# Performance work log

Measured on AMD Instinct MI355X. Metric: run time of the kernel, lower is better.

The kernel has to match this reference:

```python
import jax, jax.numpy as jnp
import numpy as np
import math

B, S, D, H, DFF = 16, 1024, 512, 8, 2048
DH = D // H
EPS = 1e-5


def setup_inputs() -> dict:
    key = jax.random.key(0)
    ks = jax.random.split(key, 16)
    sc = 0.02
    inp = {
        "x": jax.random.normal(ks[0], (B, S, D), dtype=jnp.float32),
        "mask": jnp.zeros((B, 1, 1, S), dtype=jnp.float32),
        # attention projections (stored as [in, out])
        "wq": jax.random.normal(ks[1], (D, D), jnp.float32) * sc,
        "bq": jnp.zeros((D,), jnp.float32),
        "wk": jax.random.normal(ks[2], (D, D), jnp.float32) * sc,
        "bk": jnp.zeros((D,), jnp.float32),
        "wv": jax.random.normal(ks[3], (D, D), jnp.float32) * sc,
        "bv": jnp.zeros((D,), jnp.float32),
        "wo": jax.random.normal(ks[4], (D, D), jnp.float32) * sc,
        "bo": jnp.zeros((D,), jnp.float32),
        # FFN
        "w1": jax.random.normal(ks[5], (D, DFF), jnp.float32) * sc,
        "b1": jnp.zeros((DFF,), jnp.float32),
        "w2": jax.random.normal(ks[6], (DFF, D), jnp.float32) * sc,
        "b2": jnp.zeros((D,), jnp.float32),
        # LayerNorms over the full [S, D] slab (normalized_shape=[S, D])
        "ln1_w": jnp.ones((S, D), jnp.float32),
        "ln1_b": jnp.zeros((S, D), jnp.float32),
        "ln2_w": jnp.ones((S, D), jnp.float32),
        "ln2_b": jnp.zeros((S, D), jnp.float32),
    }
    return inp


def _layernorm_2d(x, w, b):
    # torch nn.LayerNorm([S, D]): normalize jointly over last two dims
    m = jnp.mean(x, axis=(-2, -1), keepdims=True)
    v = jnp.mean(jnp.square(x - m), axis=(-2, -1), keepdims=True)
    return (x - m) * jax.lax.rsqrt(v + EPS) * w + b


def _encoder_layer(x, mask, wq, bq, wk, bk, wv, bv, wo, bo,
                   w1, b1, w2, b2, ln1_w, ln1_b, ln2_w, ln2_b):
    # --- multi-head attention ---
    def heads(t):  # [B,S,D] -> [B,H,S,DH]
        return t.reshape(B, S, H, DH).transpose(0, 2, 1, 3)

    q = heads(x @ wq + bq)
    k = heads(x @ wk + bk)
    v = heads(x @ wv + bv)

    logits = jnp.einsum("bhqd,bhkd->bhqk", q, k) / math.sqrt(DH)
    logits = logits + mask * -1e9
    attn = jax.nn.softmax(logits, axis=-1)          # [B,H,S,S]
    ctx = jnp.einsum("bhqk,bhkd->bhqd", attn, v)    # [B,H,S,DH]
    ctx = ctx.transpose(0, 2, 1, 3).reshape(B, S, D)
    attn_out = ctx @ wo + bo

    out1 = _layernorm_2d(x + attn_out, ln1_w, ln1_b)

    # --- FFN ---
    ffn = jax.nn.relu(out1 @ w1 + b1) @ w2 + b2
    out2 = _layernorm_2d(out1 + ffn, ln2_w, ln2_b)
    return out2


def reference(x, mask, wq, bq, wk, bk, wv, bv, wo, bo,
              w1, b1, w2, b2, ln1_w, ln1_b, ln2_w, ln2_b):
    return _encoder_layer(x, mask, wq, bq, wk, bk, wv, bv, wo, bo,
                          w1, b1, w2, b2, ln1_w, ln1_b, ln2_w, ln2_b)
```

## Files before the change

kernel.cpp:

```cpp
#include <hip/hip_runtime.h>
#include <stdint.h>

#define B_   16
#define S_   1024
#define D_   512
#define H_   8
#define DH_  64
#define DFF_ 2048
#define M_   (B_*S_)
#define SD_  (S_*D_)
#define NT_  16

typedef unsigned short u16;
typedef unsigned int u32;
typedef __attribute__((ext_vector_type(2))) unsigned int u32x2;
typedef __attribute__((ext_vector_type(4))) unsigned short u16x4;
typedef __attribute__((ext_vector_type(8))) short bf16x8;
typedef __attribute__((ext_vector_type(4))) float f32x4;
typedef __attribute__((ext_vector_type(16))) float f32x16;

#define LOG2E 1.4426950408889634f

#if defined(__has_builtin)
#if __has_builtin(__builtin_amdgcn_permlane32_swap)
#define HAVE_PLS 1
#endif
#endif

__device__ __forceinline__ u16 f2bf(float f) {
  union { float f; uint32_t u; } x{f};
  uint32_t r = x.u + 0x7fffu + ((x.u >> 16) & 1u);
  return (u16)(r >> 16);
}

__device__ __forceinline__ float bf2f(u16 v) {
  union { uint32_t u; float f; } x{(uint32_t)v << 16};
  return x.f;
}

__device__ __forceinline__ u32 pk2(float lo, float hi) {
  union { float f; u32 u; } a{lo}, b{hi};
  return __builtin_amdgcn_perm(b.u, a.u, 0x07060302u);
}

__device__ __forceinline__ float exp2fast(float x) {
#if __has_builtin(__builtin_amdgcn_exp2f)
  return __builtin_amdgcn_exp2f(x);
#else
  return exp2f(x);
#endif
}

__device__ __forceinline__ void gload16(const u16* g, u16* l) {
  __builtin_amdgcn_global_load_lds(
      (const __attribute__((address_space(1))) uint32_t*)g,
      (__attribute__((address_space(3))) uint32_t*)l, 16, 0, 0);
}

__device__ __forceinline__ int swz3(int r) { return (r & 7) ^ ((r >> 3) & 7); }

__global__ __launch_bounds__(256) void prep_kernel(
    const float* __restrict__ x, u16* __restrict__ xb,
    const float* __restrict__ wq, const float* __restrict__ wk,
    const float* __restrict__ wv, const float* __restrict__ wo,
    const float* __restrict__ w1, const float* __restrict__ w2,
    u16* __restrict__ wqkvT, u16* __restrict__ woT,
    u16* __restrict__ w1T, u16* __restrict__ w2T) {
  int bid = blockIdx.x, tid = threadIdx.x;
  if (bid < 8192) {
    int i = bid * 256 + tid;
    f32x4 v = ((const f32x4*)x)[i];
    u16x4 o = { f2bf(v[0]), f2bf(v[1]), f2bf(v[2]), f2bf(v[3]) };
    ((u16x4*)xb)[i] = o;
    return;
  }
  bid -= 8192;
  const float* W; u16* WT; int K, N, bx, by;
  if (bid < 1024) {
    int which = bid >> 8;
    W  = (which == 0) ? wq : (which == 1) ? wk : (which == 2) ? wv : wo;
    WT = (which == 3) ? woT : (wqkvT + (size_t)which * 512 * 512);
    K = 512; N = 512;
    int r = bid & 255; bx = r & 15; by = r >> 4;
  } else if (bid < 2048) {
    int r = bid - 1024; W = w1; WT = w1T; K = 512; N = 2048;
    bx = r & 63; by = r >> 6;
  } else {
    int r = bid - 2048; W = w2; WT = w2T; K = 2048; N = 512;
    bx = r & 15; by = r >> 4;
  }
  __shared__ float t[32][33];
  int n0 = bx * 32, k0 = by * 32;
  int tx = tid & 31, ty = tid >> 5;
  #pragma unroll
  for (int i = 0; i < 4; i++)
    t[ty + 8*i][tx] = W[(size_t)(k0 + ty + 8*i) * N + n0 + tx];
  __syncthreads();
  #pragma unroll
  for (int i = 0; i < 4; i++)
    WT[(size_t)(n0 + ty + 8*i) * K + k0 + tx] = f2bf(t[tx][ty + 8*i]);
}

template<int MODE, bool RELU>
__global__ __launch_bounds__(512, 2) void gemm256_kernel(
    const u16* __restrict__ A, const u16* __restrict__ WT,
    const float* __restrict__ bias0, const float* __restrict__ bias1,
    const float* __restrict__ bias2,
    u16* __restrict__ out0, u16* __restrict__ out1, u16* __restrict__ out2,
    int K, int ostride, int nx, int ypg) {
  __shared__ u16 lA[2][16384];
  __shared__ u16 lB[2][16384];
  int tid = threadIdx.x, lane = tid & 63;
  int wid = tid >> 6, wm = wid >> 2, wn = wid & 3;
  int l16 = lane & 15, kg4 = lane >> 4;

  int d = blockIdx.x;
  int c = d & 7, j = d >> 3;
  int x = j % nx, y = c * ypg + j / nx;
  int m0 = y * 256, n0 = x * 256;

  const u16* agp = A  + (size_t)m0 * K;
  const u16* bgp = WT + (size_t)n0 * K;
  int srow = tid >> 3, sslot = tid & 7;

  f32x4 z = {0.f, 0.f, 0.f, 0.f};
  f32x4 acc[8][4];
  #pragma unroll
  for (int mg = 0; mg < 8; mg++)
    #pragma unroll
    for (int ni = 0; ni < 4; ni++) acc[mg][ni] = z;

#define STAGE256(buf, kt) do { \
    _Pragma("unroll") \
    for (int h = 0; h < 2; h++) \
      _Pragma("unroll") \
      for (int i = 0; i < 2; i++) { \
        int r_ = h*128 + i*64 + srow; \
        int gc_ = (kt) + ((sslot ^ swz3(r_)) << 3); \
        gload16(agp + (size_t)r_ * K + gc_, &lA[buf][h*8192 + (i*512 + tid)*8]); \
        gload16(bgp + (size_t)r_ * K + gc_, &lB[buf][h*8192 + (i*512 + tid)*8]); \
      } \
  } while (0)

  int nk = K / 64;
  int cur = 0;
  STAGE256(0, 0);

  for (int t = 0; t < nk; t++) {
    __syncthreads();
    if (t + 1 < nk) STAGE256(cur ^ 1, (t + 1) * 64);
    bf16x8 bfv[4][2];
    #pragma unroll
    for (int ni = 0; ni < 4; ni++)
      #pragma unroll
      for (int kf = 0; kf < 2; kf++) {
        int row = wn*64 + ni*16 + l16;
        int slot = (kf*4 + kg4) ^ swz3(row);
        bfv[ni][kf] = *(const bf16x8*)&lB[cur][row*64 + slot*8];
      }
    #pragma unroll
    for (int p = 0; p < 4; p++) {
      bf16x8 af[2][2];
      #pragma unroll
      for (int mi = 0; mi < 2; mi++)
        #pragma unroll
        for (int kf = 0; kf < 2; kf++) {
          int row = wm*128 + p*32 + mi*16 + l16;
          int slot = (kf*4 + kg4) ^ swz3(row);
          af[mi][kf] = *(const bf16x8*)&lA[cur][row*64 + slot*8];
        }
      __builtin_amdgcn_s_setprio(1);
      #pragma unroll
      for (int kf = 0; kf < 2; kf++)
        #pragma unroll
        for (int mi = 0; mi < 2; mi++)
          #pragma unroll
          for (int ni = 0; ni < 4; ni++)
            acc[p*2 + mi][ni] = __builtin_amdgcn_mfma_f32_16x16x32_bf16(
                af[mi][kf], bfv[ni][kf], acc[p*2 + mi][ni], 0, 0, 0);
      __builtin_amdgcn_s_setprio(0);
      __builtin_amdgcn_sched_barrier(0);
    }
    cur ^= 1;
  }
#undef STAGE256

  int segbase = n0 + wn*64;
  int seg = segbase >> 9;
  const float* bp = (MODE == 2) ? (seg == 0 ? bias0 : (seg == 1 ? bias1 : bias2)) : bias0;
  u16* op = (MODE == 2) ? (seg == 0 ? out0 : (seg == 1 ? out1 : out2)) : out0;
  float aeff = (MODE == 2 && seg == 0) ? 0.125f * LOG2E : 1.0f;

  #pragma unroll
  for (int mg = 0; mg < 8; mg++)
    #pragma unroll
    for (int ni = 0; ni < 4; ni++) {
      int col = segbase + ni*16 + l16;
      int ocol = (MODE == 2) ? (col & 511) : col;
      float bv = bp[ocol];
      #pragma unroll
      for (int r = 0; r < 4; r++) {
        int row = m0 + wm*128 + mg*16 + kg4*4 + r;
        float v = (acc[mg][ni][r] + bv) * aeff;
        if (RELU) v = fmaxf(v, 0.f);
        op[(size_t)row * ostride + ocol] = f2bf(v);
      }
    }
}

template<int MODE, bool RELU, bool RESB>
__global__ __launch_bounds__(256) void gemm_kernel(
    const u16* __restrict__ A, const u16* __restrict__ WT,
    const float* __restrict__ bias0, const float* __restrict__ res,
    const u16* __restrict__ resB,
    u16* __restrict__ out0,
    float* __restrict__ partOut, int K, int N, int nx, int ypg) {
  __shared__ u16 lA[2][128 * 32];
  __shared__ u16 lB[2][128 * 32];
  __shared__ float lred[8];
  int tid = threadIdx.x;
  int lane = tid & 63, wid = tid >> 6;
  int wr = wid >> 1, wc = wid & 1;
  int lrow = lane & 15, kg = lane >> 4;

  int dd = blockIdx.x;
  int cc = dd & 7, jj = dd >> 3;
  int bx = jj % nx, by = cc * ypg + jj / nx;
  int m0 = by * 128, n0 = bx * 128;

  int r0 = tid >> 2, c0 = (tid & 3) * 8;
  const u16* agp = A  + (size_t)m0 * K;
  const u16* bgp = WT + (size_t)n0 * K;

  f32x4 z = {0.f, 0.f, 0.f, 0.f};
  f32x4 acc[4][4];
  #pragma unroll
  for (int mi = 0; mi < 4; mi++)
    #pragma unroll
    for (int ni = 0; ni < 4; ni++) acc[mi][ni] = z;

#define STAGE_G(buf, kt) do { \
    gload16(agp + (size_t)r0 * K + (kt) + c0,        &lA[buf][tid * 8]); \
    gload16(agp + (size_t)(r0 + 64) * K + (kt) + c0, &lA[buf][2048 + tid * 8]); \
    gload16(bgp + (size_t)r0 * K + (kt) + c0,        &lB[buf][tid * 8]); \
    gload16(bgp + (size_t)(r0 + 64) * K + (kt) + c0, &lB[buf][2048 + tid * 8]); \
  } while (0)

  STAGE_G(0, 0);

  int nk = K / 32;
  int cur = 0;
  for (int t = 0; t < nk; t++) {
    __syncthreads();
    if (t + 1 < nk) STAGE_G(cur ^ 1, (t + 1) * 32);
    bf16x8 af[4], bfv[4];
    #pragma unroll
    for (int mi = 0; mi < 4; mi++)
      af[mi] = *(const bf16x8*)&lA[cur][(wr*64 + mi*16 + lrow) * 32 + kg*8];
    #pragma unroll
    for (int ni = 0; ni < 4; ni++)
      bfv[ni] = *(const bf16x8*)&lB[cur][(wc*64 + ni*16 + lrow) * 32 + kg*8];
    __builtin_amdgcn_s_setprio(1);
    #pragma unroll
    for (int mi = 0; mi < 4; mi++)
      #pragma unroll
      for (int ni = 0; ni < 4; ni++)
        acc[mi][ni] = __builtin_amdgcn_mfma_f32_16x16x32_bf16(af[mi], bfv[ni], acc[mi][ni], 0, 0, 0);
    __builtin_amdgcn_s_setprio(0);
    cur ^= 1;
  }
#undef STAGE_G

  float s_acc = 0.f, q_acc = 0.f;
  #pragma unroll
  for (int mi = 0; mi < 4; mi++)
    #pragma unroll
    for (int ni = 0; ni < 4; ni++) {
      int col = n0 + wc*64 + ni*16 + lrow;
      float bv = bias0[col];
      #pragma unroll
      for (int r = 0; r < 4; r++) {
        int row = m0 + wr*64 + mi*16 + kg*4 + r;
        float v = acc[mi][ni][r] + bv;
        if (RELU) v = fmaxf(v, 0.f);
        size_t off = (size_t)row * N + col;
        if (MODE == 1) {
          float rv = RESB ? bf2f(resB[off]) : res[off];
          float tv = v + rv;
          out0[off] = f2bf(tv);
          s_acc += tv;
          q_acc += tv * tv;
        } else {
          out0[off] = f2bf(v);
        }
      }
    }

  if (MODE == 1) {
    #pragma unroll
    for (int dsh = 1; dsh < 64; dsh <<= 1) {
      s_acc += __shfl_xor(s_acc, dsh);
      q_acc += __shfl_xor(q_acc, dsh);
    }
    if (lane == 0) { lred[wid*2] = s_acc; lred[wid*2+1] = q_acc; }
    __syncthreads();
    if (tid == 0) {
      int batch = by >> 3;
      int pidx = batch*32 + (by & 7)*nx + bx;
      partOut[pidx*2]   = lred[0]+lred[2]+lred[4]+lred[6];
      partOut[pidx*2+1] = lred[1]+lred[3]+lred[5]+lred[7];
    }
  }
}

__global__ __launch_bounds__(256) void attn_kernel(
    const u16* __restrict__ Q, const u16* __restrict__ Km,
    const u16* __restrict__ Vm, const float* __restrict__ mask,
    u16* __restrict__ ctx) {
  __shared__ u16 lK[2][4096];
  __shared__ u16 lV[2][4096];
  __shared__ float lBias[1024];
  int tid = threadIdx.x, lane = tid & 63, wid = tid >> 6;
  int la = lane & 31, hi = lane >> 5;
  int wg = blockIdx.x;
  int xcd = wg & 7, idx = wg >> 3;
  int bh = xcd * 16 + (idx & 15);
  int qt = idx >> 4;
  int b = bh >> 3, h = bh & 7;

  const u16* qp = Q + (size_t)(b*S_ + qt*128 + wid*32 + la) * D_ + h*DH_ + hi*8;
  bf16x8 qf[4];
  #pragma unroll
  for (int c = 0; c < 4; c++) qf[c] = *(const bf16x8*)(qp + c*16);

  int krow = tid >> 3;
  int kcol = 8 * (tid & 7);
  int kc0 = kcol ^ (swz3(krow) << 3);
  int kc1 = kcol ^ (swz3(krow + 32) << 3);
  int va = tid & 7, vp = tid >> 3;
  const u16* kbase = Km + ((size_t)b*S_) * D_ + h*DH_;
  const u16* vbase = Vm + ((size_t)b*S_) * D_ + h*DH_ + 8*va;

#define STAGE_K(buf, tt) do { \
    const u16* kt_ = kbase + (size_t)(tt)*64*D_; \
    gload16(kt_ + (size_t)krow*D_ + kc0,        &lK[buf][tid*8]); \
    gload16(kt_ + (size_t)(krow+32)*D_ + kc1,   &lK[buf][2048 + tid*8]); \
  } while (0)
#define LOAD_V(tt) do { \
    const u16* vt_ = vbase + (size_t)((tt)*64 + 2*vp) * D_; \
    nv0 = *(const bf16x8*)vt_; nv1 = *(const bf16x8*)(vt_ + D_); \
  } while (0)
#define WRITE_V(buf) do { \
    u32* lVd_ = (u32*)lV[buf]; \
    _Pragma("unroll") \
    for (int jv = 0; jv < 8; jv++) { \
      int row_ = 8*va + jv; \
      u32 pv_ = (u32)(u16)nv0[jv] | ((u32)(u16)nv1[jv] << 16); \
      lVd_[row_*32 + (vp ^ (swz3(row_) << 2))] = pv_; \
    } \
  } while (0)

  {
    f32x4 mv = ((const f32x4*)(mask + (size_t)b*S_))[tid];
    f32x4 bv;
    #pragma unroll
    for (int jj = 0; jj < 4; jj++) bv[jj] = mv[jj] * (-1.0e9f * LOG2E);
    ((f32x4*)lBias)[tid] = bv;
  }

  int swk0 = swz3(la) << 2, swk1 = swz3(la + 32) << 2;
  f32x16 oc0, oc1;
  #pragma unroll
  for (int i = 0; i < 16; i++) { oc0[i] = 0.f; oc1[i] = 0.f; }
  float lsum = 0.f;

#define QKT(d0, d1, tt) do { \
    _Pragma("unroll") \
    for (int rq = 0; rq < 4; rq++) { \
      f32x4 bb0 = *(const f32x4*)&lBias[(tt)*64 + rq*8 + hi*4]; \
      f32x4 bb1 = *(const f32x4*)&lBias[(tt)*64 + 32 + rq*8 + hi*4]; \
      _Pragma("unroll") \
      for (int jj = 0; jj < 4; jj++) { d0[rq*4+jj] = bb0[jj]; d1[rq*4+jj] = bb1[jj]; } \
    } \
    { const u16* lkb_ = lK[(tt)&1]; \
      __builtin_amdgcn_s_setprio(1); \
      _Pragma("unroll") \
      for (int c_ = 0; c_ < 4; c_++) { \
        int dwb_ = c_*8 + hi*4; \
        bf16x8 kf0_ = *(const bf16x8*)&lkb_[la*64 + ((dwb_ ^ swk0) << 1)]; \
        bf16x8 kf1_ = *(const bf16x8*)&lkb_[(la+32)*64 + ((dwb_ ^ swk1) << 1)]; \
        d0 = __builtin_amdgcn_mfma_f32_32x32x16_bf16(kf0_, qf[c_], d0, 0, 0, 0); \
        d1 = __builtin_amdgcn_mfma_f32_32x32x16_bf16(kf1_, qf[c_], d1, 0, 0, 0); \
      } \
      __builtin_amdgcn_s_setprio(0); } \
  } while (0)

#define SOFTPV(s0v, s1v, tt) do { \
    float rsp_[4] = {0.f, 0.f, 0.f, 0.f}; \
    _Pragma("unroll") \
    for (int i_ = 0; i_ < 16; i_++) { float e_ = exp2fast(s0v[i_]); s0v[i_] = e_; rsp_[i_ & 3] += e_; } \
    _Pragma("unroll") \
    for (int i_ = 0; i_ < 16; i_++) { float e_ = exp2fast(s1v[i_]); s1v[i_] = e_; rsp_[i_ & 3] += e_; } \
    lsum += (rsp_[0] + rsp_[1]) + (rsp_[2] + rsp_[3]); \
    { const u16* lvb_ = lV[(tt)&1]; \
      __builtin_amdgcn_s_setprio(1); \
      _Pragma("unroll") \
      for (int cc_ = 0; cc_ < 4; cc_++) { \
        const int base_ = 8 * (cc_ & 1); \
        float pv_[8]; \
        _Pragma("unroll") \
        for (int k_ = 0; k_ < 8; k_++) pv_[k_] = (cc_ < 2) ? s0v[base_ + k_] : s1v[base_ + k_]; \
        u32 a0_ = pk2(pv_[0], pv_[1]); \
        u32 a1_ = pk2(pv_[2], pv_[3]); \
        u32 b0_ = pk2(pv_[4], pv_[5]); \
        u32 b1_ = pk2(pv_[6], pv_[7]); \
        union { u32 u[4]; bf16x8 v; } pf_; \
        PEXCH(pf_, a0_, a1_, b0_, b1_); \
        _Pragma("unroll") \
        for (int vb_ = 0; vb_ < 2; vb_++) { \
          int row_ = vb_*32 + la; \
          int dwv_ = (cc_*8 + hi*4) ^ (swz3(row_) << 2); \
          bf16x8 vf_ = *(const bf16x8*)&lvb_[row_*64 + (dwv_ << 1)]; \
          if (vb_ == 0) oc0 = __builtin_amdgcn_mfma_f32_32x32x16_bf16(pf_.v, vf_, oc0, 0, 0, 0); \
          else          oc1 = __builtin_amdgcn_mfma_f32_32x32x16_bf16(pf_.v, vf_, oc1, 0, 0, 0); \
        } \
      } \
      __builtin_amdgcn_s_setprio(0); } \
  } while (0)

#ifdef HAVE_PLS
#define PEXCH(pf_, a0_, a1_, b0_, b1_) do { \
    u32x2 r0_ = __builtin_amdgcn_permlane32_swap(a0_, b0_, false, false); \
    u32x2 r1_ = __builtin_amdgcn_permlane32_swap(a1_, b1_, false, false); \
    pf_.u[0] = r0_[0]; pf_.u[1] = r1_[0]; pf_.u[2] = r0_[1]; pf_.u[3] = r1_[1]; \
  } while (0)
#else
#define PEXCH(pf_, a0_, a1_, b0_, b1_) do { \
    u32 sd0_ = hi ? a0_ : b0_, sd1_ = hi ? a1_ : b1_; \
    u32 x0_ = (u32)__shfl_xor((int)sd0_, 32); \
    u32 x1_ = (u32)__shfl_xor((int)sd1_, 32); \
    pf_.u[0] = hi ? x0_ : a0_; \
    pf_.u[1] = hi ? x1_ : a1_; \
    pf_.u[2] = hi ? b0_ : x0_; \
    pf_.u[3] = hi ? b1_ : x1_; \
  } while (0)
#endif

  bf16x8 nv0, nv1;
  STAGE_K(0, 0);
  LOAD_V(0);
  WRITE_V(0);
  LOAD_V(1);
  STAGE_K(1, 1);
  __syncthreads();

  f32x16 sA0, sA1, sB0, sB1;
  QKT(sA0, sA1, 0);
  __syncthreads();

  for (int t = 0; t < NT_; t += 2) {
    if (t + 2 < NT_) STAGE_K(t & 1, t + 2);
    WRITE_V((t + 1) & 1);
    if (t + 2 < NT_) LOAD_V(t + 2);
    QKT(sB0, sB1, t + 1);
    SOFTPV(sA0, sA1, t);
    __syncthreads();
    {
      int u = t + 1;
      if (u + 2 < NT_) STAGE_K(u & 1, u + 2);
      if (u + 1 < NT_) WRITE_V((u + 1) & 1);
      if (u + 2 < NT_) LOAD_V(u + 2);
      if (u + 1 < NT_) QKT(sA0, sA1, u + 1);
      SOFTPV(sB0, sB1, u);
      __syncthreads();
    }
  }
#undef STAGE_K
#undef LOAD_V
#undef WRITE_V
#undef QKT
#undef SOFTPV
#undef PEXCH

  lsum += __shfl_xor(lsum, 32);
  float linv = 1.f / lsum;
  #pragma unroll
  for (int r = 0; r < 16; r++) {
    int qr = (r&3) + 8*(r>>2) + 4*hi;
    float lr = __shfl(linv, qr);
    size_t rowoff = (size_t)(b*S_ + qt*128 + wid*32 + qr) * D_ + h*DH_;
    ctx[rowoff + la]      = f2bf(oc0[r] * lr);
    ctx[rowoff + 32 + la] = f2bf(oc1[r] * lr);
  }
}

template<bool WB, bool WF>
__global__ __launch_bounds__(256) void ln_apply_kernel(
    const u16* __restrict__ r, const float* __restrict__ part,
    const float* __restrict__ w, const float* __restrict__ bb,
    float* __restrict__ outF, u16* __restrict__ outB) {
  int b = blockIdx.y, c = blockIdx.x, tid = threadIdx.x;
  float s = 0.f, q = 0.f;
  for (int i = 0; i < 32; i++) { s += part[(b*32+i)*2]; q += part[(b*32+i)*2+1]; }
  const float inv = 1.f / (float)SD_;
  float mean = s * inv;
  float var = q * inv - mean * mean;
  float rs = rsqrtf(var + 1e-5f);
  size_t base = (size_t)b * SD_;
  #pragma unroll
  for (int i = 0; i < 8; i++) {
    int li4 = c*2048 + i*256 + tid;
    u16x4 rv = ((const u16x4*)(r + base))[li4];
    f32x4 wv = ((const f32x4*)w)[li4];
    f32x4 bv = ((const f32x4*)bb)[li4];
    f32x4 ov;
    #pragma unroll
    for (int jj = 0; jj < 4; jj++) ov[jj] = (bf2f(rv[jj]) - mean) * rs * wv[jj] + bv[jj];
    if (WF) ((f32x4*)(outF + base))[li4] = ov;
    if (WB) {
      u16x4 ub = { f2bf(ov[0]), f2bf(ov[1]), f2bf(ov[2]), f2bf(ov[3]) };
      ((u16x4*)(outB + base))[li4] = ub;
    }
  }
}

extern "C" void kernel_launch(void* const* d_in, const int* in_sizes, int n_in,
                              void* d_out, int out_size, void* d_ws, size_t ws_size,
                              hipStream_t stream) {
  (void)in_sizes; (void)n_in; (void)out_size; (void)ws_size;
  const float* x    = (const float*)d_in[0];
  const float* mask = (const float*)d_in[1];
  const float* wq = (const float*)d_in[2];
  const float* bq = (const float*)d_in[3];
  const float* wk = (const float*)d_in[4];
  const float* bk = (const float*)d_in[5];
  const float* wv = (const float*)d_in[6];
  const float* bv = (const float*)d_in[7];
  const float* wo = (const float*)d_in[8];
  const float* bo = (const float*)d_in[9];
  const float* w1 = (const float*)d_in[10];
  const float* b1 = (const float*)d_in[11];
  const float* w2 = (const float*)d_in[12];
  const float* b2 = (const float*)d_in[13];
  const float* ln1w = (const float*)d_in[14];
  const float* ln1b = (const float*)d_in[15];
  const float* ln2w = (const float*)d_in[16];
  const float* ln2b = (const float*)d_in[17];
  float* out = (float*)d_out;

  char* ws = (char*)d_ws;
  const size_t MB = 1ull << 20;
  u16*   xb    = (u16*)(ws + 0);
  u16*   Qb    = (u16*)(ws + 16*MB);
  u16*   Kb    = (u16*)(ws + 32*MB);
  u16*   Vb    = (u16*)(ws + 48*MB);
  u16*   ctxb  = (u16*)(ws + 64*MB);
  u16*   res1b = (u16*)(ws + 80*MB);
  u16*   out1b = (u16*)(ws + 0);
  u16*   ffn1  = (u16*)(ws + 16*MB);
  u16*   res2b = (u16*)(ws + 112*MB);
  float* part  = (float*)(ws + 144*MB);
  u16*   wqkvT = (u16*)(ws + 145*MB);
  u16*   woT   = (u16*)(ws + 147*MB);
  u16*   w1T   = (u16*)(ws + 148*MB);
  u16*   w2T   = (u16*)(ws + 150*MB);

  prep_kernel<<<11264, 256, 0, stream>>>(
      x, xb, wq, wk, wv, wo, w1, w2, wqkvT, woT, w1T, w2T);

  gemm256_kernel<2,false><<<384, 512, 0, stream>>>(
      xb, wqkvT, bq, bk, bv, Qb, Kb, Vb, 512, 512, 6, 8);

  attn_kernel<<<1024, 256, 0, stream>>>(Qb, Kb, Vb, mask, ctxb);

  gemm_kernel<1,false,true><<<512, 256, 0, stream>>>(
      ctxb, woT, bo, nullptr, xb, res1b, part, 512, 512, 4, 16);

  ln_apply_kernel<true,false><<<dim3(64,16), 256, 0, stream>>>(
      res1b, part, ln1w, ln1b, nullptr, out1b);

  gemm256_kernel<0,true><<<512, 512, 0, stream>>>(
      out1b, w1T, b1, nullptr, nullptr, ffn1, nullptr, nullptr, 512, 2048, 8, 8);

  gemm_kernel<1,false,true><<<512, 256, 0, stream>>>(
      ffn1, w2T, b2, nullptr, out1b, res2b, part, 2048, 512, 4, 16);

  ln_apply_kernel<false,true><<<dim3(64,16), 256, 0, stream>>>(
      res2b, part, ln2w, ln2b, out, nullptr);
}
```

Measured before the change: 244.8 us.

## Replace 256x256 GEMM kernel with 128x128 tiles for QKV and FFN1

Removes the 512-thread 256x256-tile GEMM and runs the QKV projection with a new 128x128-tile, 256-thread kernel (1536 blocks) and FFN1 with the existing 128-tile gemm_kernel (2048 blocks). Smaller tiles give more blocks and better occupancy and tail balance across CUs. In exchange each block reuses less data per load, so more global and LDS traffic goes through a K-step of 32 with no LDS swizzle, which risks bank conflicts and lower MFMA utilisation.

```diff
diff --git a/kernel.cpp b/kernel.cpp
--- a/kernel.cpp
+++ b/kernel.cpp
@@ -99,113 +99,6 @@
   #pragma unroll
   for (int i = 0; i < 4; i++)
     WT[(size_t)(n0 + ty + 8*i) * K + k0 + tx] = f2bf(t[tx][ty + 8*i]);
-}
-
-template<int MODE, bool RELU>
-__global__ __launch_bounds__(512, 2) void gemm256_kernel(
-    const u16* __restrict__ A, const u16* __restrict__ WT,
-    const float* __restrict__ bias0, const float* __restrict__ bias1,
-    const float* __restrict__ bias2,
-    u16* __restrict__ out0, u16* __restrict__ out1, u16* __restrict__ out2,
-    int K, int ostride, int nx, int ypg) {
-  __shared__ u16 lA[2][16384];
-  __shared__ u16 lB[2][16384];
-  int tid = threadIdx.x, lane = tid & 63;
-  int wid = tid >> 6, wm = wid >> 2, wn = wid & 3;
-  int l16 = lane & 15, kg4 = lane >> 4;
-
-  int d = blockIdx.x;
-  int c = d & 7, j = d >> 3;
-  int x = j % nx, y = c * ypg + j / nx;
-  int m0 = y * 256, n0 = x * 256;
-
-  const u16* agp = A  + (size_t)m0 * K;
-  const u16* bgp = WT + (size_t)n0 * K;
-  int srow = tid >> 3, sslot = tid & 7;
-
-  f32x4 z = {0.f, 0.f, 0.f, 0.f};
-  f32x4 acc[8][4];
-  #pragma unroll
-  for (int mg = 0; mg < 8; mg++)
-    #pragma unroll
-    for (int ni = 0; ni < 4; ni++) acc[mg][ni] = z;
-
-#define STAGE256(buf, kt) do { \
-    _Pragma("unroll") \
-    for (int h = 0; h < 2; h++) \
-      _Pragma("unroll") \
-      for (int i = 0; i < 2; i++) { \
-        int r_ = h*128 + i*64 + srow; \
-        int gc_ = (kt) + ((sslot ^ swz3(r_)) << 3); \
-        gload16(agp + (size_t)r_ * K + gc_, &lA[buf][h*8192 + (i*512 + tid)*8]); \
-        gload16(bgp + (size_t)r_ * K + gc_, &lB[buf][h*8192 + (i*512 + tid)*8]); \
-      } \
-  } while (0)
-
-  int nk = K / 64;
-  int cur = 0;
-  STAGE256(0, 0);
-
-  for (int t = 0; t < nk; t++) {
-    __syncthreads();
-    if (t + 1 < nk) STAGE256(cur ^ 1, (t + 1) * 64);
-    bf16x8 bfv[4][2];
-    #pragma unroll
-    for (int ni = 0; ni < 4; ni++)
-      #pragma unroll
-      for (int kf = 0; kf < 2; kf++) {
-        int row = wn*64 + ni*16 + l16;
-        int slot = (kf*4 + kg4) ^ swz3(row);
-        bfv[ni][kf] = *(const bf16x8*)&lB[cur][row*64 + slot*8];
-      }
-    #pragma unroll
-    for (int p = 0; p < 4; p++) {
-      bf16x8 af[2][2];
-      #pragma unroll
-      for (int mi = 0; mi < 2; mi++)
-        #pragma unroll
-        for (int kf = 0; kf < 2; kf++) {
-          int row = wm*128 + p*32 + mi*16 + l16;
-          int slot = (kf*4 + kg4) ^ swz3(row);
-          af[mi][kf] = *(const bf16x8*)&lA[cur][row*64 + slot*8];
-        }
-      __builtin_amdgcn_s_setprio(1);
-      #pragma unroll
-      for (int kf = 0; kf < 2; kf++)
-        #pragma unroll
-        for (int mi = 0; mi < 2; mi++)
-          #pragma unroll
-          for (int ni = 0; ni < 4; ni++)
-            acc[p*2 + mi][ni] = __builtin_amdgcn_mfma_f32_16x16x32_bf16(
-                af[mi][kf], bfv[ni][kf], acc[p*2 + mi][ni], 0, 0, 0);
-      __builtin_amdgcn_s_setprio(0);
-      __builtin_amdgcn_sched_barrier(0);
-    }
-    cur ^= 1;
-  }
-#undef STAGE256
-
-  int segbase = n0 + wn*64;
-  int seg = segbase >> 9;
-  const float* bp = (MODE == 2) ? (seg == 0 ? bias0 : (seg == 1 ? bias1 : bias2)) : bias0;
-  u16* op = (MODE == 2) ? (seg == 0 ? out0 : (seg == 1 ? out1 : out2)) : out0;
-  float aeff = (MODE == 2 && seg == 0) ? 0.125f * LOG2E : 1.0f;
-
-  #pragma unroll
-  for (int mg = 0; mg < 8; mg++)
-    #pragma unroll
-    for (int ni = 0; ni < 4; ni++) {
-      int col = segbase + ni*16 + l16;
-      int ocol = (MODE == 2) ? (col & 511) : col;
-      float bv = bp[ocol];
-      #pragma unroll
-      for (int r = 0; r < 4; r++) {
-        int row = m0 + wm*128 + mg*16 + kg4*4 + r;
-        float v = (acc[mg][ni][r] + bv) * aeff;
-        if (RELU) v = fmaxf(v, 0.f);
-        op[(size_t)row * ostride + ocol] = f2bf(v);
-      }
-    }
 }
 
 template<int MODE, bool RELU, bool RESB>
@@ -311,6 +204,88 @@
       partOut[pidx*2+1] = lred[1]+lred[3]+lred[5]+lred[7];
     }
   }
+}
+
+__global__ __launch_bounds__(256) void gemm128_qkv_kernel(
+    const u16* __restrict__ A, const u16* __restrict__ WT,
+    const float* __restrict__ bq, const float* __restrict__ bk,
+    const float* __restrict__ bv,
+    u16* __restrict__ Qb, u16* __restrict__ Kb, u16* __restrict__ Vb,
+    int K, int nx, int ypg) {
+  __shared__ u16 lA[2][128 * 32];
+  __shared__ u16 lB[2][128 * 32];
+  int tid = threadIdx.x;
+  int lane = tid & 63, wid = tid >> 6;
+  int wr = wid >> 1, wc = wid & 1;
+  int lrow = lane & 15, kg = lane >> 4;
+
+  int dd = blockIdx.x;
+  int cc = dd & 7, jj = dd >> 3;
+  int bx = jj % nx, by = cc * ypg + jj / nx;
+  int m0 = by * 128, n0 = bx * 128;
+
+  int r0 = tid >> 2, c0 = (tid & 3) * 8;
+  const u16* agp = A  + (size_t)m0 * K;
+  const u16* bgp = WT + (size_t)n0 * K;
+
+  f32x4 z = {0.f, 0.f, 0.f, 0.f};
+  f32x4 acc[4][4];
+  #pragma unroll
+  for (int mi = 0; mi < 4; mi++)
+    #pragma unroll
+    for (int ni = 0; ni < 4; ni++) acc[mi][ni] = z;
+
+#define STAGE_G(buf, kt) do { \
+    gload16(agp + (size_t)r0 * K + (kt) + c0,        &lA[buf][tid * 8]); \
+    gload16(agp + (size_t)(r0 + 64) * K + (kt) + c0, &lA[buf][2048 + tid * 8]); \
+    gload16(bgp + (size_t)r0 * K + (kt) + c0,        &lB[buf][tid * 8]); \
+    gload16(bgp + (size_t)(r0 + 64) * K + (kt) + c0, &lB[buf][2048 + tid * 8]); \
+  } while (0)
+
+  STAGE_G(0, 0);
+
+  int nk = K / 32;
+  int cur = 0;
+  for (int t = 0; t < nk; t++) {
+    __syncthreads();
+    if (t + 1 < nk) STAGE_G(cur ^ 1, (t + 1) * 32);
+    bf16x8 af[4], bfv[4];
+    #pragma unroll
+    for (int mi = 0; mi < 4; mi++)
+      af[mi] = *(const bf16x8*)&lA[cur][(wr*64 + mi*16 + lrow) * 32 + kg*8];
+    #pragma unroll
+    for (int ni = 0; ni < 4; ni++)
+      bfv[ni] = *(const bf16x8*)&lB[cur][(wc*64 + ni*16 + lrow) * 32 + kg*8];
+    __builtin_amdgcn_s_setprio(1);
+    #pragma unroll
+    for (int mi = 0; mi < 4; mi++)
+      #pragma unroll
+      for (int ni = 0; ni < 4; ni++)
+        acc[mi][ni] = __builtin_amdgcn_mfma_f32_16x16x32_bf16(af[mi], bfv[ni], acc[mi][ni], 0, 0, 0);
+    __builtin_amdgcn_s_setprio(0);
+    cur ^= 1;
+  }
+#undef STAGE_G
+
+  int seg = n0 >> 9;
+  const float* bp = (seg == 0) ? bq : (seg == 1) ? bk : bv;
+  u16* op = (seg == 0) ? Qb : (seg == 1) ? Kb : Vb;
+  float aeff = (seg == 0) ? 0.125f * LOG2E : 1.0f;
+
+  #pragma unroll
+  for (int mi = 0; mi < 4; mi++)
+    #pragma unroll
+    for (int ni = 0; ni < 4; ni++) {
+      int col = n0 + wc*64 + ni*16 + lrow;
+      int ocol = col & 511;
+      float bvv = bp[ocol];
+      #pragma unroll
+      for (int r = 0; r < 4; r++) {
+        int row = m0 + wr*64 + mi*16 + kg*4 + r;
+        float v = (acc[mi][ni][r] + bvv) * aeff;
+        op[(size_t)row * 512 + ocol] = f2bf(v);
+      }
+    }
 }
 
 __global__ __launch_bounds__(256) void attn_kernel(
@@ -568,8 +543,8 @@
   prep_kernel<<<11264, 256, 0, stream>>>(
       x, xb, wq, wk, wv, wo, w1, w2, wqkvT, woT, w1T, w2T);
 
-  gemm256_kernel<2,false><<<384, 512, 0, stream>>>(
-      xb, wqkvT, bq, bk, bv, Qb, Kb, Vb, 512, 512, 6, 8);
+  gemm128_qkv_kernel<<<1536, 256, 0, stream>>>(
+      xb, wqkvT, bq, bk, bv, Qb, Kb, Vb, 512, 12, 16);
 
   attn_kernel<<<1024, 256, 0, stream>>>(Qb, Kb, Vb, mask, ctxb);
 
@@ -579,8 +554,8 @@
   ln_apply_kernel<true,false><<<dim3(64,16), 256, 0, stream>>>(
       res1b, part, ln1w, ln1b, nullptr, out1b);
 
-  gemm256_kernel<0,true><<<512, 512, 0, stream>>>(
-      out1b, w1T, b1, nullptr, nullptr, ffn1, nullptr, nullptr, 512, 2048, 8, 8);
+  gemm_kernel<0,true,false><<<2048, 256, 0, stream>>>(
+      out1b, w1T, b1, nullptr, nullptr, ffn1, nullptr, 512, 2048, 16, 16);
 
   gemm_kernel<1,false,true><<<512, 256, 0, stream>>>(
       ffn1, w2T, b2, nullptr, out1b, res2b, part, 2048, 512, 4, 16);
```

New measurement: 235.6 us, median of 2. -3.8%, faster.
